# Kernel optimization log

Measured on AMD Instinct MI355X. Metric: run time of the kernel, lower is better.

The kernel has to match this reference:

```python
import jax, jax.numpy as jnp
import numpy as np

N_NODES = 2048
UNITS = 64
IN_DIM = 64
K_DIFF = 2  # max_diffusion_step


def _rw_norm_t(adj):
    # random-walk normalize D^{-1}(A+I), then transpose (as in forward())
    a = adj + jnp.eye(adj.shape[0], dtype=adj.dtype)
    d = jnp.sum(a, axis=1)
    d_inv = jnp.where(d > 0, 1.0 / jnp.where(d > 0, d, 1.0), 0.0)
    return (d_inv[:, None] * a).T


def _gconv(x_cat, adj_t, W, b):
    # x_cat: (B, N, F). Chebyshev-like diffusion: x0, A x0, 2 A x1 - x0, ...
    x0 = x_cat
    xs = [x0]
    x1 = jnp.einsum('nm,bmf->bnf', adj_t, x0)
    xs.append(x1)
    for _ in range(2, K_DIFF + 1):
        x2 = 2.0 * jnp.einsum('nm,bmf->bnf', adj_t, x1) - x0
        xs.append(x2)
        x0, x1 = x1, x2
    x = jnp.stack(xs, axis=-1)  # (B, N, F, K+1) -> matches torch permute(3,1,2,0)
    B, N, F, K = x.shape
    x = x.reshape(B * N, F * K)
    out = x @ W + b
    return out.reshape(B, N, -1)


def setup_inputs() -> dict:
    key = jax.random.key(0)
    ks = jax.random.split(key, 6)
    B = 64
    inputs = jax.random.normal(ks[0], (B, N_NODES * IN_DIM), dtype=jnp.float32)
    hx = jax.random.normal(ks[1], (B, N_NODES * UNITS), dtype=jnp.float32)
    adj = jax.random.uniform(ks[2], (N_NODES, N_NODES), dtype=jnp.float32)
    in_sz = IN_DIM + UNITS
    nm = K_DIFF + 1
    scale = float(np.sqrt(2.0 / (in_sz * nm + 2 * UNITS)))  # xavier-ish
    W_ru = jax.random.normal(ks[3], (in_sz * nm, 2 * UNITS), dtype=jnp.float32) * scale
    b_ru = jnp.ones((2 * UNITS,), dtype=jnp.float32)  # bias_start=1.0
    W_c = jax.random.normal(ks[4], (in_sz * nm, UNITS), dtype=jnp.float32) * scale
    b_c = jnp.zeros((UNITS,), dtype=jnp.float32)
    return {"inputs": inputs, "hx": hx, "adj": adj,
            "W_ru": W_ru, "b_ru": b_ru, "W_c": W_c, "b_c": b_c}


def reference(inputs, hx, adj, W_ru, b_ru, W_c, b_c):
    B = inputs.shape[0]
    x = inputs.reshape(B, N_NODES, IN_DIM)
    h = hx.reshape(B, N_NODES, UNITS)
    adj_t = _rw_norm_t(adj)
    # r/u gates via graph conv + sigmoid
    ru = jax.nn.sigmoid(_gconv(jnp.concatenate([x, h], axis=-1), adj_t, W_ru, b_ru))
    r, u = ru[..., :UNITS], ru[..., UNITS:]
    # candidate state
    c = jnp.tanh(_gconv(jnp.concatenate([x, r * h], axis=-1), adj_t, W_c, b_c))
    new_state = u * h + (1.0 - u) * c
    return new_state.reshape(B, N_NODES * UNITS)
```

## Files before the change

### kernel.cpp

```cpp
#include <hip/hip_runtime.h>
#include <math.h>

typedef __attribute__((ext_vector_type(8))) short short8;
typedef __attribute__((ext_vector_type(4))) float float4v;
typedef __attribute__((ext_vector_type(16))) float float16v;
typedef __attribute__((ext_vector_type(4))) unsigned short ushort4v;
typedef unsigned short u16;
typedef unsigned int u32;

#define NB 64
#define NN 2048
#define FD 128
#define UD 64
#define KT 384


__device__ __forceinline__ u16 f2bf(float f) {
    unsigned int u = __float_as_uint(f);
    u += 0x7fffu + ((u >> 16) & 1u);
    return (u16)(u >> 16);
}
__device__ __forceinline__ float bf2f(u16 s) {
    return __uint_as_float(((unsigned int)s) << 16);
}
__device__ __forceinline__ float sigmoidf_(float x) {
    return 1.0f / (1.0f + expf(-x));
}
__device__ __forceinline__ void gl2lds16(const u16* g, u16* l) {
    __builtin_amdgcn_global_load_lds((const __attribute__((address_space(1))) unsigned int*)g,
                                     (__attribute__((address_space(3))) unsigned int*)l,
                                     16, 0, 0);
}

__global__ void k_prep(const float* __restrict__ adj, float* __restrict__ d_inv,
                       const float* __restrict__ W_ru, u16* __restrict__ Wru,
                       const float* __restrict__ W_c,  u16* __restrict__ Wc,
                       const float* __restrict__ x, const float* __restrict__ h,
                       u16* __restrict__ X0f, u16* __restrict__ X0m) {
    __shared__ u16 T[128 * 136];
    int bid = blockIdx.x;
    int t = threadIdx.x;
    if (bid < 2048) {
        int m = bid;
        const float4v* row = (const float4v*)(adj + (size_t)m * NN);
        float s = 0.f;
        for (int i = t; i < NN / 4; i += 256) {
            float4v v = row[i];
            s += v.x + v.y + v.z + v.w;
        }
        float* red = (float*)T;
        for (int off = 32; off; off >>= 1) s += __shfl_down(s, off, 64);
        if ((t & 63) == 0) red[t >> 6] = s;
        __syncthreads();
        if (t == 0) {
            float tt = red[0] + red[1] + red[2] + red[3] + 1.0f;
            d_inv[m] = 1.0f / tt;
        }
        return;
    }
    if (bid < 2336) {
        const float* W; u16* Wt; int OD, idx;
        if (bid < 2240) { W = W_ru; Wt = Wru; OD = FD; idx = (bid - 2048) * 256 + t; }
        else            { W = W_c;  Wt = Wc;  OD = UD; idx = (bid - 2240) * 256 + t; }
        if (idx >= KT * OD) return;
        int o  = idx % OD;
        int kp = idx / OD;
        int kd = kp >> 7, f = kp & 127;
        float v;
        if (kd == 0)      v = W[(size_t)(f * 3 + 0) * OD + o] - W[(size_t)(f * 3 + 2) * OD + o];
        else if (kd == 1) v = W[(size_t)(f * 3 + 1) * OD + o];
        else              v = 2.0f * W[(size_t)(f * 3 + 2) * OD + o];
        size_t dst = ((size_t)(o >> 5) * 12 + (kp >> 5)) * 1024 + (((kp >> 3) & 3) * 32 + (o & 31)) * 8 + (kp & 7);
        Wt[dst] = f2bf(v);
        return;
    }
    int rb = bid - 2336;
    int m0 = (rb & 15) * 128;
    int b  = rb >> 4;
    const float* srcs[2] = { x + (size_t)b * (NN * 64), h + (size_t)b * (NN * 64) };
    for (int s = 0; s < 2; ++s) {
        const float* src = srcs[s];
        for (int p = 0; p < 8; ++p) {
            int idx = t + 256 * p;
            int mi = idx >> 4;
            int f4 = idx & 15;
            float4v v = *(const float4v*)(src + (size_t)(m0 + mi) * 64 + f4 * 4);
            float vv[4] = {v.x, v.y, v.z, v.w};
#pragma unroll
            for (int j = 0; j < 4; ++j)
                T[(s * 64 + f4 * 4 + j) * 136 + mi] = f2bf(vv[j]);
        }
    }
    __syncthreads();
#pragma unroll
    for (int p = 0; p < 8; ++p) {
        int S = t + 256 * p;
        int fgl = S >> 9, kgl = (S >> 7) & 3, s = S & 127;
        int c = s >> 5, r = s & 31;
        short8 v = *(const short8*)(T + (fgl * 32 + r) * 136 + kgl * 32 + c * 8);
        *(short8*)(X0f + ((size_t)(b * 4 + fgl) * 64 + (m0 >> 5) + kgl) * 1024 + s * 8) = v;
    }
#pragma unroll
    for (int p = 0; p < 8; ++p) {
        int S = t + 256 * p;
        int fc = S >> 7;
        int mi = S & 127;
        short8 v;
#pragma unroll
        for (int e = 0; e < 8; ++e) v[e] = (short)T[(fc * 8 + e) * 136 + mi];
        size_t dst = ((size_t)(b * 64 + (m0 >> 5) + (mi >> 5)) * 4 + (fc >> 2)) * 1024
                     + ((fc & 3) * 32 + (mi & 31)) * 8;
        *(short8*)(X0m + dst) = v;
    }
}

__global__ void k_adjT(const float* __restrict__ adj, const float* __restrict__ d_inv,
                       u16* __restrict__ adjT) {
    __shared__ u16 T[64 * 72];
    int m0 = blockIdx.x * 64;
    int n0 = blockIdx.y * 64;
    int t = threadIdx.x;
    for (int p = 0; p < 4; ++p) {
        int idx = t + 256 * p;
        int i  = idx >> 4;
        int n4 = idx & 15;
        int m = m0 + i;
        float4v v = *(const float4v*)(adj + (size_t)m * NN + n0 + n4 * 4);
        float di = d_inv[m];
        float vv[4] = {v.x, v.y, v.z, v.w};
#pragma unroll
        for (int j = 0; j < 4; ++j) {
            int n = n0 + n4 * 4 + j;
            float a = vv[j] + ((m == n) ? 1.0f : 0.0f);
            T[(n4 * 4 + j) * 72 + i] = f2bf(a * di);
        }
    }
    __syncthreads();
#pragma unroll
    for (int p = 0; p < 2; ++p) {
        int S = t + 256 * p;
        int rgl = S >> 8, kgl = (S >> 7) & 1, s = S & 127;
        int c = s >> 5, r = s & 31;
        short8 v = *(const short8*)(T + (rgl * 32 + r) * 72 + kgl * 32 + c * 8);
        *(short8*)(adjT + ((size_t)((n0 >> 5) + rgl) * 64 + (m0 >> 5) + kgl) * 1024 + s * 8) = v;
    }
}

#define GSTEP(KT, W0, W1, W2, W3, L0, L1, L2, L3)                              \
  {                                                                            \
    if ((KT) + 3 < 64) {                                                       \
      size_t ko = (size_t)((KT) + 3) * 1024;                                   \
      L0 = *(const short8*)(gA[0] + ko);                                       \
      L1 = *(const short8*)(gA[1] + ko);                                       \
      L2 = *(const short8*)(gB[0] + ko);                                       \
      L3 = *(const short8*)(gB[1] + ko);                                       \
    }                                                                          \
    __builtin_amdgcn_sched_barrier(0);                                         \
    if ((KT) + 2 < 64) {                                                       \
      u16* wb = SM + bW * 16384;                                               \
      *(short8*)(wb + la[0]) = W0;                                             \
      *(short8*)(wb + la[1]) = W1;                                             \
      *(short8*)(wb + lb[0]) = W2;                                             \
      *(short8*)(wb + lb[1]) = W3;                                             \
    }                                                                          \
    u16* rb_ = SM + bR * 16384;                                                \
    short8 fa[4], fb[2];                                                       \
    _Pragma("unroll") for (int mt = 0; mt < 4; ++mt)                           \
      fa[mt] = *(const short8*)(rb_ + rdA + mt * 1024);                        \
    _Pragma("unroll") for (int nt = 0; nt < 2; ++nt)                           \
      fb[nt] = *(const short8*)(rb_ + rdB + nt * 1024);                        \
    __builtin_amdgcn_s_setprio(1);                                             \
    _Pragma("unroll") for (int mt = 0; mt < 4; ++mt)                           \
      _Pragma("unroll") for (int nt = 0; nt < 2; ++nt)                         \
        acc[mt][nt] = __builtin_amdgcn_mfma_f32_32x32x16_bf16(fa[mt], fb[nt], acc[mt][nt], 0, 0, 0); \
    __builtin_amdgcn_s_setprio(0);                                             \
    _Pragma("unroll") for (int mt = 0; mt < 4; ++mt)                           \
      fa[mt] = *(const short8*)(rb_ + rdA + mt * 1024 + 512);                  \
    _Pragma("unroll") for (int nt = 0; nt < 2; ++nt)                           \
      fb[nt] = *(const short8*)(rb_ + rdB + nt * 1024 + 512);                  \
    __builtin_amdgcn_s_setprio(1);                                             \
    _Pragma("unroll") for (int mt = 0; mt < 4; ++mt)                           \
      _Pragma("unroll") for (int nt = 0; nt < 2; ++nt)                         \
        acc[mt][nt] = __builtin_amdgcn_mfma_f32_32x32x16_bf16(fa[mt], fb[nt], acc[mt][nt], 0, 0, 0); \
    __builtin_amdgcn_s_setprio(0);                                             \
    asm volatile("s_waitcnt lgkmcnt(0)" ::: "memory");                         \
    if ((KT) < 63) {                                                           \
      __builtin_amdgcn_s_barrier();                                            \
      __builtin_amdgcn_sched_barrier(0);                                       \
    }                                                                          \
    bR = (bR == 2) ? 0 : bR + 1;                                               \
    bW = (bW == 2) ? 0 : bW + 1;                                               \
  }

template<int HAS_F>
__global__ __launch_bounds__(512, 2)
void k_gemm256(const u16* __restrict__ Ap, const u16* __restrict__ Bc,
               u16* __restrict__ outF, u16* __restrict__ outM) {
    __shared__ __align__(16) u16 SM[49152];
    int bid = blockIdx.x;
    int wxcd = bid >> 3;
    int cb = (bid & 7) * 4 + (wxcd & 3);
    int nb = wxcd >> 2;
    int n0 = nb * 256, c0 = cb * 256;
    int t = threadIdx.x;
    int wave = t >> 6, lane = t & 63;
    int wx = wave >> 2;
    int wy = wave & 3;
    int ln = lane & 31, hi = lane >> 5;

    const u16* gA[2];
    const u16* gB[2];
    int la[2], lb[2];
#pragma unroll
    for (int i = 0; i < 2; ++i) {
        int idx = i * 512 + t;
        int p = idx >> 7, s = idx & 127;
        gA[i] = Bc + ((size_t)((c0 >> 5) + p) * 64) * 1024 + s * 8;
        gB[i] = Ap + ((size_t)((n0 >> 5) + p) * 64) * 1024 + s * 8;
        la[i] = idx * 8;
        lb[i] = 8192 + idx * 8;
    }

    float16v acc[4][2];
#pragma unroll
    for (int mt = 0; mt < 4; ++mt)
#pragma unroll
        for (int nt = 0; nt < 2; ++nt)
#pragma unroll
            for (int e = 0; e < 16; ++e) acc[mt][nt][e] = 0.f;

    int rdA = wx * 4096 + lane * 8;
    int rdB = 8192 + wy * 2048 + lane * 8;

    short8 PA0, PA1, PA2, PA3, QB0, QB1, QB2, QB3;
    PA0 = *(const short8*)(gA[0]);        PA1 = *(const short8*)(gA[1]);
    PA2 = *(const short8*)(gB[0]);        PA3 = *(const short8*)(gB[1]);
    QB0 = *(const short8*)(gA[0] + 1024); QB1 = *(const short8*)(gA[1] + 1024);
    QB2 = *(const short8*)(gB[0] + 1024); QB3 = *(const short8*)(gB[1] + 1024);
    *(short8*)(SM + la[0]) = PA0; *(short8*)(SM + la[1]) = PA1;
    *(short8*)(SM + lb[0]) = PA2; *(short8*)(SM + lb[1]) = PA3;
    asm volatile("s_waitcnt lgkmcnt(0)" ::: "memory");
    PA0 = *(const short8*)(gA[0] + 2048); PA1 = *(const short8*)(gA[1] + 2048);
    PA2 = *(const short8*)(gB[0] + 2048); PA3 = *(const short8*)(gB[1] + 2048);
    *(short8*)(SM + 16384 + la[0]) = QB0; *(short8*)(SM + 16384 + la[1]) = QB1;
    *(short8*)(SM + 16384 + lb[0]) = QB2; *(short8*)(SM + 16384 + lb[1]) = QB3;
    asm volatile("s_waitcnt lgkmcnt(0)" ::: "memory");
    __builtin_amdgcn_s_barrier();
    __builtin_amdgcn_sched_barrier(0);

    int bR = 0, bW = 2;
    for (int i = 0; i < 32; ++i) {
        GSTEP(2 * i,     PA0, PA1, PA2, PA3, QB0, QB1, QB2, QB3);
        GSTEP(2 * i + 1, QB0, QB1, QB2, QB3, PA0, PA1, PA2, PA3);
    }

    int batch0 = cb * 2 + wx;
#pragma unroll
    for (int mt = 0; mt < 4; ++mt) {
#pragma unroll
        for (int nt = 0; nt < 2; ++nt) {
            int mg = (n0 >> 5) + wy * 2 + nt;
            size_t pbase = ((size_t)(batch0 * 64 + mg) * 4 + mt) * 1024;
#pragma unroll
            for (int eq = 0; eq < 4; ++eq) {
                ushort4v pk;
#pragma unroll
                for (int r = 0; r < 4; ++r) pk[r] = f2bf(acc[mt][nt][eq * 4 + r]);
                *(ushort4v*)(outM + pbase + (eq * 32 + ln) * 8 + 4 * hi) = pk;
            }
        }
    }

    if (HAS_F) {
#pragma unroll
        for (int p = 0; p < 2; ++p) {
            __syncthreads();
            if ((wy >> 1) == p) {
#pragma unroll
                for (int mt = 0; mt < 4; ++mt)
#pragma unroll
                    for (int nt = 0; nt < 2; ++nt)
#pragma unroll
                        for (int e = 0; e < 16; ++e) {
                            int cl = wx * 128 + mt * 32 + 4 * hi + 8 * (e >> 2) + (e & 3);
                            int nl = (wy & 1) * 64 + nt * 32 + ln;
                            SM[cl * 136 + nl] = f2bf(acc[mt][nt][e]);
                        }
            }
            __syncthreads();
#pragma unroll
            for (int j = 0; j < 8; ++j) {
                int S = t + 512 * j;
                int col = S >> 4, nd8 = S & 15;
                short8 v = *(const short8*)(SM + col * 136 + nd8 * 8);
                int gn = n0 + p * 128 + nd8 * 8;
                size_t dst = ((size_t)((c0 >> 5) + (col >> 5)) * 64 + (gn >> 5)) * 1024
                             + (size_t)((((gn >> 3) & 3) * 32 + (col & 31))) * 8;
                *(short8*)(outF + dst) = v;
            }
        }
    }
}

template<int FG>
__global__ __launch_bounds__(256, 4)
void k_gemm(const u16* __restrict__ A, const u16* __restrict__ Bc,
            u16* __restrict__ outF, u16* __restrict__ outM, int cBlocks) {
    __shared__ u16 SM[16384];
    u16* A0 = SM;            u16* A1 = SM + 4096;
    u16* B0 = SM + 8192;     u16* B1 = SM + 12288;

    int id = blockIdx.x + cBlocks * blockIdx.y;
    int band = cBlocks >> 3;
    int g = id & 7, s = id >> 3;
    int cb = g * band + (s % band);
    int nb = s / band;
    int c0 = cb * 128;
    int n0 = nb * 128;

    int t = threadIdx.x;
    int wave = t >> 6, lane = t & 63;
    int wy = wave & 1, wx = wave >> 1;
    int ln = lane & 31, hi = lane >> 5;
    int l16 = lane * 8;

    const u16* gaP[2];
    const u16* gbP[2];
#pragma unroll
    for (int i = 0; i < 2; ++i) {
        int T = t + 256 * i;
        gaP[i] = A  + ((size_t)((n0 >> 5) + (T >> 7)) * 64) * 1024 + (size_t)(T & 127) * 8;
        gbP[i] = Bc + ((size_t)((c0 >> 5) + (T >> 7)) * 64) * 1024 + (size_t)(T & 127) * 8;
    }

    float16v acc[2][2];
#pragma unroll
    for (int i = 0; i < 2; ++i)
#pragma unroll
        for (int j = 0; j < 2; ++j)
#pragma unroll
            for (int e = 0; e < 16; ++e) acc[i][j][e] = 0.f;

#pragma unroll
    for (int i = 0; i < 2; ++i) { gl2lds16(gaP[i], A0 + (t + 256 * i) * 8); gl2lds16(gbP[i], B0 + (t + 256 * i) * 8); }

#pragma unroll 2
    for (int it = 0; it < 64; ++it) {
        u16* Ac = (it & 1) ? A1 : A0;
        u16* Bs = (it & 1) ? B1 : B0;
        __syncthreads();
        if (it + 1 < 64) {
            int ko = (it + 1) * 1024;
            u16* An = (it & 1) ? A0 : A1;
            u16* Bn = (it & 1) ? B0 : B1;
#pragma unroll
            for (int i = 0; i < 2; ++i) { gl2lds16(gaP[i] + ko, An + (t + 256 * i) * 8); gl2lds16(gbP[i] + ko, Bn + (t + 256 * i) * 8); }
        }
        short8 fa[2][2], fb[2][2];
#pragma unroll
        for (int ks = 0; ks < 2; ++ks) {
#pragma unroll
            for (int mt = 0; mt < 2; ++mt)
                fa[ks][mt] = *(const short8*)(Bs + ((wx * 2 + mt) * 2 + ks) * 512 + l16);
#pragma unroll
            for (int nt = 0; nt < 2; ++nt)
                fb[ks][nt] = *(const short8*)(Ac + ((wy * 2 + nt) * 2 + ks) * 512 + l16);
        }
#pragma unroll
        for (int ks = 0; ks < 2; ++ks)
#pragma unroll
            for (int mt = 0; mt < 2; ++mt)
#pragma unroll
                for (int nt = 0; nt < 2; ++nt)
                    acc[mt][nt] = __builtin_amdgcn_mfma_f32_32x32x16_bf16(fa[ks][mt], fb[ks][nt], acc[mt][nt], 0, 0, 0);
    }

#pragma unroll
    for (int mt = 0; mt < 2; ++mt) {
#pragma unroll
        for (int nt = 0; nt < 2; ++nt) {
            int mg = (n0 >> 5) + wy * 2 + nt;
            int batch = (FG == 4) ? cb : (2 * cb + wx);
            int fg = (FG == 4) ? (wx * 2 + mt) : mt;
            size_t pbase = ((size_t)(batch * 64 + mg) * FG + fg) * 1024;
#pragma unroll
            for (int eq = 0; eq < 4; ++eq) {
                ushort4v pk;
#pragma unroll
                for (int r = 0; r < 4; ++r) pk[r] = f2bf(acc[mt][nt][eq * 4 + r]);
                *(ushort4v*)(outM + pbase + (eq * 32 + ln) * 8 + 4 * hi) = pk;
            }
        }
    }

    if (outF) {
        __syncthreads();
#pragma unroll
        for (int p = 0; p < 2; ++p) {
            if (p) __syncthreads();
            if (wx == p) {
#pragma unroll
                for (int mt = 0; mt < 2; ++mt)
#pragma unroll
                    for (int nt = 0; nt < 2; ++nt)
#pragma unroll
                        for (int e = 0; e < 16; ++e) {
                            int cl = mt * 32 + 4 * hi + 8 * (e >> 2) + (e & 3);
                            int nl = wy * 64 + nt * 32 + ln;
                            SM[cl * 136 + nl] = f2bf(acc[mt][nt][e]);
                        }
            }
            __syncthreads();
#pragma unroll
            for (int pp = 0; pp < 4; ++pp) {
                int S = t + 256 * pp;
                int rgl = S >> 9, kgl = (S >> 7) & 3, sl = S & 127;
                int c = sl >> 5, r = sl & 31;
                short8 v = *(const short8*)(SM + (rgl * 32 + r) * 136 + kgl * 32 + c * 8);
                size_t gaddr = ((size_t)((c0 >> 5) + p * 2 + rgl) * 64 + (n0 >> 5) + kgl) * 1024 + sl * 8;
                *(short8*)(outF + gaddr) = v;
            }
        }
    }
}

__global__ __launch_bounds__(256, 3)
void k_proj_ru(const u16* __restrict__ X0m, const u16* __restrict__ X1m, const u16* __restrict__ Ym,
               const u16* __restrict__ Wp, const float* __restrict__ bias, const float* __restrict__ hx,
               u16* __restrict__ RH0f, u16* __restrict__ RH0m, u16* __restrict__ Ut) {
    __shared__ u16 SM[16384];
    u16 *Xa = SM, *Xb = SM + 4096, *Wa = SM + 8192, *Wb = SM + 12288;
    int mb = blockIdx.x, b = blockIdx.y;
    int m0 = mb * 128, mg0 = mb * 4;
    int t = threadIdx.x, wave = t >> 6, lane = t & 63;
    int wx = wave & 1, wyy = wave >> 1;
    int ln = lane & 31, hi = lane >> 5;
    const u16* Xs[3] = {X0m, X1m, Ym};
    int p0 = t >> 7, s0 = t & 127;

    float16v acc[2][2];
#pragma unroll
    for (int i = 0; i < 2; ++i)
#pragma unroll
        for (int j = 0; j < 2; ++j)
#pragma unroll
            for (int e = 0; e < 16; ++e) acc[i][j][e] = 0.f;

    gl2lds16(Xs[0] + ((size_t)((b * 64 + mg0 + p0) * 4)) * 1024 + s0 * 8, Xa + t * 8);
    gl2lds16(Xs[0] + ((size_t)((b * 64 + mg0 + p0 + 2) * 4)) * 1024 + s0 * 8, Xa + (t + 256) * 8);
    gl2lds16(Wp + ((size_t)(p0 * 12)) * 1024 + s0 * 8, Wa + t * 8);
    gl2lds16(Wp + ((size_t)((p0 + 2) * 12)) * 1024 + s0 * 8, Wa + (t + 256) * 8);

    for (int kq = 0; kq < 12; ++kq) {
        u16* Xc = (kq & 1) ? Xb : Xa;
        u16* Wc = (kq & 1) ? Wb : Wa;
        __syncthreads();
        if (kq + 1 < 12) {
            int k2 = kq + 1, kd = k2 >> 2, kg = k2 & 3;
            u16* Xn = (kq & 1) ? Xa : Xb;
            u16* Wn = (kq & 1) ? Wa : Wb;
            const u16* xb = Xs[kd];
            gl2lds16(xb + ((size_t)((b * 64 + mg0 + p0) * 4 + kg)) * 1024 + s0 * 8, Xn + t * 8);
            gl2lds16(xb + ((size_t)((b * 64 + mg0 + p0 + 2) * 4 + kg)) * 1024 + s0 * 8, Xn + (t + 256) * 8);
            gl2lds16(Wp + ((size_t)(p0 * 12 + k2)) * 1024 + s0 * 8, Wn + t * 8);
            gl2lds16(Wp + ((size_t)((p0 + 2) * 12 + k2)) * 1024 + s0 * 8, Wn + (t + 256) * 8);
        }
        short8 fa[2][2], fb[2][2];
#pragma unroll
        for (int ks = 0; ks < 2; ++ks) {
#pragma unroll
            for (int mt = 0; mt < 2; ++mt)
                fa[ks][mt] = *(const short8*)(Xc + ((wx * 2 + mt) * 2 + ks) * 512 + lane * 8);
#pragma unroll
            for (int nt = 0; nt < 2; ++nt)
                fb[ks][nt] = *(const short8*)(Wc + ((wyy * 2 + nt) * 2 + ks) * 512 + lane * 8);
        }
#pragma unroll
        for (int ks = 0; ks < 2; ++ks)
#pragma unroll
            for (int mt = 0; mt < 2; ++mt)
#pragma unroll
                for (int nt = 0; nt < 2; ++nt)
                    acc[mt][nt] = __builtin_amdgcn_mfma_f32_32x32x16_bf16(fa[ks][mt], fb[ks][nt], acc[mt][nt], 0, 0, 0);
    }
    __syncthreads();
    if (wyy == 0) {
#pragma unroll
        for (int mt = 0; mt < 2; ++mt)
#pragma unroll
            for (int nt = 0; nt < 2; ++nt) {
                int o = nt * 32 + ln;
                float bo = bias[o];
                u16 vals[16];
#pragma unroll
                for (int e = 0; e < 16; ++e) {
                    int ml = wx * 64 + mt * 32 + 4 * hi + 8 * (e >> 2) + (e & 3);
                    float sg = sigmoidf_(acc[mt][nt][e] + bo);
                    float hh = hx[((size_t)b * NN + m0 + ml) * 64 + o];
                    vals[e] = f2bf(sg * hh);
                    SM[ml * 76 + o] = vals[e];
                }
#pragma unroll
                for (int eq = 0; eq < 4; ++eq) {
                    ushort4v pk;
#pragma unroll
                    for (int r = 0; r < 4; ++r) pk[r] = vals[eq * 4 + r];
                    size_t addr = ((size_t)(b * 2 + nt) * 64 + mg0 + wx * 2 + mt) * 1024 + (eq * 32 + ln) * 8 + 4 * hi;
                    *(ushort4v*)(RH0f + addr) = pk;
                }
            }
    } else {
#pragma unroll
        for (int mt = 0; mt < 2; ++mt)
#pragma unroll
            for (int nt = 0; nt < 2; ++nt) {
                int og = nt * 32 + ln;
                float bo = bias[64 + og];
#pragma unroll
                for (int e = 0; e < 16; ++e) {
                    int ml = wx * 64 + mt * 32 + 4 * hi + 8 * (e >> 2) + (e & 3);
                    Ut[((size_t)b * NN + m0 + ml) * 64 + og] = f2bf(sigmoidf_(acc[mt][nt][e] + bo));
                }
            }
    }
    __syncthreads();
#pragma unroll
    for (int j = 0; j < 4; ++j) {
        int C = t + 256 * j;
        int p = C >> 7, sl = C & 127;
        int mgl = p >> 1, ug = p & 1;
        int cq = sl >> 5, r = sl & 31;
        short8 v = *(const short8*)(SM + (mgl * 32 + r) * 76 + ug * 32 + cq * 8);
        *(short8*)(RH0m + ((size_t)((b * 64 + mg0 + mgl) * 2 + ug)) * 1024 + sl * 8) = v;
    }
}

__global__ __launch_bounds__(256, 4)
void k_proj_c(const u16* __restrict__ X0m, const u16* __restrict__ X1m, const u16* __restrict__ Ym,
              const u16* __restrict__ RH0m, const u16* __restrict__ RH1m, const u16* __restrict__ Zm,
              const u16* __restrict__ Wp, const float* __restrict__ bias,
              const float* __restrict__ hx, const u16* __restrict__ Ut,
              float* __restrict__ out) {
    __shared__ u16 SM[12288];
    u16 *Xa = SM, *Xb = SM + 4096, *Wa = SM + 8192, *Wb = SM + 10240;
    int mb = blockIdx.x, b = blockIdx.y;
    int m0 = mb * 128, mg0 = mb * 4;
    int t = threadIdx.x, wave = t >> 6, lane = t & 63;
    int wx = wave & 1, wyy = wave >> 1;
    int ln = lane & 31, hi = lane >> 5;
    const u16* Xs[3] = {X0m, X1m, Ym};
    const u16* Rs[3] = {RH0m, RH1m, Zm};
    int p0 = t >> 7, s0 = t & 127;

    float16v acc[2];
#pragma unroll
    for (int i = 0; i < 2; ++i)
#pragma unroll
        for (int e = 0; e < 16; ++e) acc[i][e] = 0.f;

    gl2lds16(Xs[0] + ((size_t)((b * 64 + mg0 + p0) * 4)) * 1024 + s0 * 8, Xa + t * 8);
    gl2lds16(Xs[0] + ((size_t)((b * 64 + mg0 + p0 + 2) * 4)) * 1024 + s0 * 8, Xa + (t + 256) * 8);
    gl2lds16(Wp + ((size_t)(p0 * 12)) * 1024 + s0 * 8, Wa + t * 8);

    for (int kq = 0; kq < 12; ++kq) {
        u16* Xc = (kq & 1) ? Xb : Xa;
        u16* Wc = (kq & 1) ? Wb : Wa;
        __syncthreads();
        if (kq + 1 < 12) {
            int k2 = kq + 1, kd = k2 >> 2, fb2 = (k2 & 3) * 32;
            u16* Xn = (kq & 1) ? Xa : Xb;
            u16* Wn = (kq & 1) ? Wa : Wb;
            const u16* mat; size_t pb0, pb1;
            if (fb2 < 64) {
                mat = Xs[kd];
                pb0 = ((size_t)((b * 64 + mg0 + p0) * 4 + (fb2 >> 5))) * 1024;
                pb1 = ((size_t)((b * 64 + mg0 + p0 + 2) * 4 + (fb2 >> 5))) * 1024;
            } else {
                mat = Rs[kd];
                pb0 = ((size_t)((b * 64 + mg0 + p0) * 2 + ((fb2 >> 5) - 2))) * 1024;
                pb1 = ((size_t)((b * 64 + mg0 + p0 + 2) * 2 + ((fb2 >> 5) - 2))) * 1024;
            }
            gl2lds16(mat + pb0 + s0 * 8, Xn + t * 8);
            gl2lds16(mat + pb1 + s0 * 8, Xn + (t + 256) * 8);
            gl2lds16(Wp + ((size_t)(p0 * 12 + k2)) * 1024 + s0 * 8, Wn + t * 8);
        }
        short8 fa[2][2], fbg[2];
#pragma unroll
        for (int ks = 0; ks < 2; ++ks) {
#pragma unroll
            for (int mt = 0; mt < 2; ++mt)
                fa[ks][mt] = *(const short8*)(Xc + ((wx * 2 + mt) * 2 + ks) * 512 + lane * 8);
            fbg[ks] = *(const short8*)(Wc + (wyy * 2 + ks) * 512 + lane * 8);
        }
#pragma unroll
        for (int ks = 0; ks < 2; ++ks)
#pragma unroll
            for (int mt = 0; mt < 2; ++mt)
                acc[mt] = __builtin_amdgcn_mfma_f32_32x32x16_bf16(fa[ks][mt], fbg[ks], acc[mt], 0, 0, 0);
    }
    int o = wyy * 32 + ln;
    float bo = bias[o];
#pragma unroll
    for (int mt = 0; mt < 2; ++mt)
#pragma unroll
        for (int e = 0; e < 16; ++e) {
            int ml = wx * 64 + mt * 32 + 4 * hi + 8 * (e >> 2) + (e & 3);
            size_t idx = ((size_t)b * NN + m0 + ml) * 64 + o;
            float c = tanhf(acc[mt][e] + bo);
            float u = bf2f(Ut[idx]);
            float hh = hx[idx];
            out[idx] = u * hh + (1.0f - u) * c;
        }
}

extern "C" void kernel_launch(void* const* d_in, const int* in_sizes, int n_in,
                              void* d_out, int out_size, void* d_ws, size_t ws_size,
                              hipStream_t stream) {
    const float* x    = (const float*)d_in[0];
    const float* hx   = (const float*)d_in[1];
    const float* adj  = (const float*)d_in[2];
    const float* W_ru = (const float*)d_in[3];
    const float* b_ru = (const float*)d_in[4];
    const float* W_c  = (const float*)d_in[5];
    const float* b_c  = (const float*)d_in[6];
    float* out = (float*)d_out;

    char* ws = (char*)d_ws;
    size_t off = 0;
    auto alloc = [&](size_t bytes) -> void* {
        void* p = ws + off;
        off += (bytes + 255) & ~(size_t)255;
        return p;
    };
    float* d_inv = (float*)alloc((size_t)NN * 4);
    u16* adjT = (u16*)alloc((size_t)NN * NN * 2);
    u16* Wru  = (u16*)alloc((size_t)FD * KT * 2);
    u16* Wc   = (u16*)alloc((size_t)UD * KT * 2);
    u16* X0f = (u16*)alloc((size_t)NB * FD * NN * 2);
    u16* X1f = (u16*)alloc((size_t)NB * FD * NN * 2);
    u16* X0m = (u16*)alloc((size_t)NB * FD * NN * 2);
    u16* X1m = (u16*)alloc((size_t)NB * FD * NN * 2);
    u16* Ym  = (u16*)alloc((size_t)NB * FD * NN * 2);
    u16* RH0m = (u16*)alloc((size_t)NB * UD * NN * 2);
    u16* RH1m = (u16*)alloc((size_t)NB * UD * NN * 2);
    u16* Zm   = (u16*)alloc((size_t)NB * UD * NN * 2);
    u16* Ut   = (u16*)alloc((size_t)NB * UD * NN * 2);
    u16* RH0f = X0f;
    u16* RH1f = X1f;

    k_prep<<<dim3(3360), dim3(256), 0, stream>>>(adj, d_inv, W_ru, Wru, W_c, Wc, x, hx, X0f, X0m);
    k_adjT<<<dim3(32, 32), dim3(256), 0, stream>>>(adj, d_inv, adjT);
    k_gemm256<1><<<dim3(256), dim3(512), 0, stream>>>(adjT, X0f, X1f, X1m);
    k_gemm256<0><<<dim3(256), dim3(512), 0, stream>>>(adjT, X1f, nullptr, Ym);
    k_proj_ru<<<dim3(16, NB), dim3(256), 0, stream>>>(X0m, X1m, Ym, Wru, b_ru, hx, RH0f, RH0m, Ut);
    k_gemm<2><<<dim3(32, 16), dim3(256), 0, stream>>>(adjT, RH0f, RH1f, RH1m, 32);
    k_gemm<2><<<dim3(32, 16), dim3(256), 0, stream>>>(adjT, RH1f, nullptr, Zm, 32);
    k_proj_c<<<dim3(16, NB), dim3(256), 0, stream>>>(X0m, X1m, Ym, RH0m, RH1m, Zm, Wc, b_c, hx, Ut, out);
}
```

Baseline: 441.0 us.

## Load B fragments directly to registers and stream A via direct global-to-LDS loads

The GEMM main loop now reads the adjacency (B) operand fragments straight from global memory into registers per wave, skipping the LDS round trip, since each wave's B fragments are private to that wave. The shared A operand is moved with direct global-to-LDS loads into a 4-deep ring buffer, synchronised with vmcnt waits instead of register staging and lgkmcnt waits. This removes LDS writes and reads for B and shrinks LDS use, at the cost of redundant global reads of B across waves sharing wy, and more delicate counter-based synchronisation.

New measurement: 446.9 us. About the same (+1.4%).

```diff
diff --git a/kernel.cpp b/kernel.cpp
--- a/kernel.cpp
+++ b/kernel.cpp
@@ -146,57 +146,54 @@
     }
 }
 
-#define GSTEP(KT, W0, W1, W2, W3, L0, L1, L2, L3)                              \
+#define GSTEP5(KT, C00, C01, C10, C11, N00, N01, N10, N11)                     \
   {                                                                            \
-    if ((KT) + 3 < 64) {                                                       \
+    if ((KT) < 63) {                                                           \
+      size_t fo = (size_t)((KT) + 1) * 1024;                                   \
+      N00 = *(const short8*)(gF0 + fo);                                        \
+      N01 = *(const short8*)(gF0 + fo + 512);                                  \
+      N10 = *(const short8*)(gF1 + fo);                                        \
+      N11 = *(const short8*)(gF1 + fo + 512);                                  \
+    }                                                                          \
+    if ((KT) < 61) {                                                           \
       size_t ko = (size_t)((KT) + 3) * 1024;                                   \
-      L0 = *(const short8*)(gA[0] + ko);                                       \
-      L1 = *(const short8*)(gA[1] + ko);                                       \
-      L2 = *(const short8*)(gB[0] + ko);                                       \
-      L3 = *(const short8*)(gB[1] + ko);                                       \
+      u16* sb = SM + (((KT) + 3) & 3) * 8192;                                  \
+      gl2lds16(gA[0] + ko, sb + la[0]);                                        \
+      gl2lds16(gA[1] + ko, sb + la[1]);                                        \
     }                                                                          \
     __builtin_amdgcn_sched_barrier(0);                                         \
-    if ((KT) + 2 < 64) {                                                       \
-      u16* wb = SM + bW * 16384;                                               \
-      *(short8*)(wb + la[0]) = W0;                                             \
-      *(short8*)(wb + la[1]) = W1;                                             \
-      *(short8*)(wb + lb[0]) = W2;                                             \
-      *(short8*)(wb + lb[1]) = W3;                                             \
-    }                                                                          \
-    u16* rb_ = SM + bR * 16384;                                                \
-    short8 fa[4], fb[2];                                                       \
+    u16* rb_ = SM + ((KT) & 3) * 8192;                                         \
+    short8 fa[4];                                                              \
     _Pragma("unroll") for (int mt = 0; mt < 4; ++mt)                           \
       fa[mt] = *(const short8*)(rb_ + rdA + mt * 1024);                        \
-    _Pragma("unroll") for (int nt = 0; nt < 2; ++nt)                           \
-      fb[nt] = *(const short8*)(rb_ + rdB + nt * 1024);                        \
     __builtin_amdgcn_s_setprio(1);                                             \
-    _Pragma("unroll") for (int mt = 0; mt < 4; ++mt)                           \
-      _Pragma("unroll") for (int nt = 0; nt < 2; ++nt)                         \
-        acc[mt][nt] = __builtin_amdgcn_mfma_f32_32x32x16_bf16(fa[mt], fb[nt], acc[mt][nt], 0, 0, 0); \
+    _Pragma("unroll") for (int mt = 0; mt < 4; ++mt) {                         \
+      acc[mt][0] = __builtin_amdgcn_mfma_f32_32x32x16_bf16(fa[mt], C00, acc[mt][0], 0, 0, 0); \
+      acc[mt][1] = __builtin_amdgcn_mfma_f32_32x32x16_bf16(fa[mt], C10, acc[mt][1], 0, 0, 0); \
+    }                                                                          \
     __builtin_amdgcn_s_setprio(0);                                             \
     _Pragma("unroll") for (int mt = 0; mt < 4; ++mt)                           \
       fa[mt] = *(const short8*)(rb_ + rdA + mt * 1024 + 512);                  \
-    _Pragma("unroll") for (int nt = 0; nt < 2; ++nt)                           \
-      fb[nt] = *(const short8*)(rb_ + rdB + nt * 1024 + 512);                  \
     __builtin_amdgcn_s_setprio(1);                                             \
-    _Pragma("unroll") for (int mt = 0; mt < 4; ++mt)                           \
-      _Pragma("unroll") for (int nt = 0; nt < 2; ++nt)                         \
-        acc[mt][nt] = __builtin_amdgcn_mfma_f32_32x32x16_bf16(fa[mt], fb[nt], acc[mt][nt], 0, 0, 0); \
+    _Pragma("unroll") for (int mt = 0; mt < 4; ++mt) {                         \
+      acc[mt][0] = __builtin_amdgcn_mfma_f32_32x32x16_bf16(fa[mt], C01, acc[mt][0], 0, 0, 0); \
+      acc[mt][1] = __builtin_amdgcn_mfma_f32_32x32x16_bf16(fa[mt], C11, acc[mt][1], 0, 0, 0); \
+    }                                                                          \
     __builtin_amdgcn_s_setprio(0);                                             \
-    asm volatile("s_waitcnt lgkmcnt(0)" ::: "memory");                         \
+    if ((KT) < 61)       asm volatile("s_waitcnt vmcnt(12)" ::: "memory");     \
+    else if ((KT) == 61) asm volatile("s_waitcnt vmcnt(10)" ::: "memory");     \
+    else if ((KT) == 62) asm volatile("s_waitcnt vmcnt(8)"  ::: "memory");     \
     if ((KT) < 63) {                                                           \
       __builtin_amdgcn_s_barrier();                                            \
       __builtin_amdgcn_sched_barrier(0);                                       \
     }                                                                          \
-    bR = (bR == 2) ? 0 : bR + 1;                                               \
-    bW = (bW == 2) ? 0 : bW + 1;                                               \
   }
 
 template<int HAS_F>
 __global__ __launch_bounds__(512, 2)
 void k_gemm256(const u16* __restrict__ Ap, const u16* __restrict__ Bc,
                u16* __restrict__ outF, u16* __restrict__ outM) {
-    __shared__ __align__(16) u16 SM[49152];
+    __shared__ __align__(16) u16 SM[34816];
     int bid = blockIdx.x;
     int wxcd = bid >> 3;
     int cb = (bid & 7) * 4 + (wxcd & 3);
@@ -209,17 +206,16 @@
     int ln = lane & 31, hi = lane >> 5;
 
     const u16* gA[2];
-    const u16* gB[2];
-    int la[2], lb[2];
+    int la[2];
 #pragma unroll
     for (int i = 0; i < 2; ++i) {
         int idx = i * 512 + t;
         int p = idx >> 7, s = idx & 127;
         gA[i] = Bc + ((size_t)((c0 >> 5) + p) * 64) * 1024 + s * 8;
-        gB[i] = Ap + ((size_t)((n0 >> 5) + p) * 64) * 1024 + s * 8;
         la[i] = idx * 8;
-        lb[i] = 8192 + idx * 8;
-    }
+    }
+    const u16* gF0 = Ap + ((size_t)((n0 >> 5) + wy * 2 + 0) * 64) * 1024 + lane * 8;
+    const u16* gF1 = Ap + ((size_t)((n0 >> 5) + wy * 2 + 1) * 64) * 1024 + lane * 8;
 
     float16v acc[4][2];
 #pragma unroll
@@ -230,28 +226,24 @@
             for (int e = 0; e < 16; ++e) acc[mt][nt][e] = 0.f;
 
     int rdA = wx * 4096 + lane * 8;
-    int rdB = 8192 + wy * 2048 + lane * 8;
-
-    short8 PA0, PA1, PA2, PA3, QB0, QB1, QB2, QB3;
-    PA0 = *(const short8*)(gA[0]);        PA1 = *(const short8*)(gA[1]);
-    PA2 = *(const short8*)(gB[0]);        PA3 = *(const short8*)(gB[1]);
-    QB0 = *(const short8*)(gA[0] + 1024); QB1 = *(const short8*)(gA[1] + 1024);
-    QB2 = *(const short8*)(gB[0] + 1024); QB3 = *(const short8*)(gB[1] + 1024);
-    *(short8*)(SM + la[0]) = PA0; *(short8*)(SM + la[1]) = PA1;
-    *(short8*)(SM + lb[0]) = PA2; *(short8*)(SM + lb[1]) = PA3;
-    asm volatile("s_waitcnt lgkmcnt(0)" ::: "memory");
-    PA0 = *(const short8*)(gA[0] + 2048); PA1 = *(const short8*)(gA[1] + 2048);
-    PA2 = *(const short8*)(gB[0] + 2048); PA3 = *(const short8*)(gB[1] + 2048);
-    *(short8*)(SM + 16384 + la[0]) = QB0; *(short8*)(SM + 16384 + la[1]) = QB1;
-    *(short8*)(SM + 16384 + lb[0]) = QB2; *(short8*)(SM + 16384 + lb[1]) = QB3;
-    asm volatile("s_waitcnt lgkmcnt(0)" ::: "memory");
+
+#pragma unroll
+    for (int tt = 0; tt < 3; ++tt) {
+        gl2lds16(gA[0] + tt * 1024, SM + tt * 8192 + la[0]);
+        gl2lds16(gA[1] + tt * 1024, SM + tt * 8192 + la[1]);
+    }
+    short8 C00, C01, C10, C11, N00, N01, N10, N11;
+    C00 = *(const short8*)(gF0);
+    C01 = *(const short8*)(gF0 + 512);
+    C10 = *(const short8*)(gF1);
+    C11 = *(const short8*)(gF1 + 512);
+    asm volatile("s_waitcnt vmcnt(8)" ::: "memory");
     __builtin_amdgcn_s_barrier();
     __builtin_amdgcn_sched_barrier(0);
 
-    int bR = 0, bW = 2;
     for (int i = 0; i < 32; ++i) {
-        GSTEP(2 * i,     PA0, PA1, PA2, PA3, QB0, QB1, QB2, QB3);
-        GSTEP(2 * i + 1, QB0, QB1, QB2, QB3, PA0, PA1, PA2, PA3);
+        GSTEP5(2 * i,     C00, C01, C10, C11, N00, N01, N10, N11);
+        GSTEP5(2 * i + 1, N00, N01, N10, N11, C00, C01, C10, C11);
     }
 
     int batch0 = cb * 2 + wx;
```
